# Kernel optimization log

Measured on AMD Instinct MI355X. Metric: run time of the kernel, lower is better.

The kernel has to match this reference:

```python
import jax, jax.numpy as jnp
import numpy as np

# DeepSeek-V3 MLA attention (q_lora_rank > 0 path), sdpa attn_type (causal)
B, S, DIM = 2, 2048, 2048
NH = 16
Q_LORA = 1536
KV_LORA = 512
NOPE = 128
ROPE = 64
VH = 128
QK_HD = NOPE + ROPE  # 192
EPS = 1e-6
SCALE = QK_HD ** -0.5
ROPE_THETA = 10000.0


def _freqs(seqlen, dim, base):
    f = 1.0 / base ** (np.arange(0, dim, 2, dtype=np.float32) / dim)
    ang = np.outer(np.arange(seqlen, dtype=np.float32), f)
    return jnp.asarray(np.cos(ang)), jnp.asarray(np.sin(ang))


def rmsnorm(x, w, eps=EPS):
    var = jnp.mean(jnp.square(x), axis=-1, keepdims=True)
    return x * jax.lax.rsqrt(var + eps) * w


def apply_rope(x, cos, sin):
    # x: [b, s, h, d]; cos/sin: [s, d//2]; interleaved complex pairs (x[2i], x[2i+1])
    xr, xi = x[..., 0::2], x[..., 1::2]
    c = cos[None, :, None, :]
    s = sin[None, :, None, :]
    yr = xr * c - xi * s
    yi = xr * s + xi * c
    return jnp.stack([yr, yi], axis=-1).reshape(x.shape)


def setup_inputs() -> dict:
    key = jax.random.key(0)
    ks = jax.random.split(key, 7)
    std = 0.02
    x = jax.random.normal(ks[0], (B, S, DIM), dtype=jnp.float32)
    cos, sin = _freqs(S, ROPE, ROPE_THETA)
    return {
        "x": x,
        "freqs_cos": cos,
        "freqs_sin": sin,
        "wq_a": jax.random.normal(ks[1], (DIM, Q_LORA), dtype=jnp.float32) * std,
        "q_norm_w": jnp.ones((Q_LORA,), dtype=jnp.float32),
        "wq_b": jax.random.normal(ks[2], (Q_LORA, NH * QK_HD), dtype=jnp.float32) * std,
        "wkv_a": jax.random.normal(ks[3], (DIM, KV_LORA + ROPE), dtype=jnp.float32) * std,
        "kv_norm_w": jnp.ones((KV_LORA,), dtype=jnp.float32),
        "wkv_b": jax.random.normal(ks[4], (KV_LORA, NH * (NOPE + VH)), dtype=jnp.float32) * std,
        "wo": jax.random.normal(ks[5], (NH * VH, DIM), dtype=jnp.float32) * std,
    }


def reference(x, freqs_cos, freqs_sin, wq_a, q_norm_w, wq_b, wkv_a, kv_norm_w, wkv_b, wo):
    b, s, _ = x.shape
    # low-rank Q projection: wq_a -> RMSNorm -> wq_b
    q = rmsnorm(x @ wq_a, q_norm_w) @ wq_b
    q = q.reshape(b, s, NH, QK_HD)
    q_nope, q_pe = q[..., :NOPE], q[..., NOPE:]
    q_pe = apply_rope(q_pe, freqs_cos, freqs_sin)
    q = jnp.concatenate([q_nope, q_pe], axis=-1)
    # low-rank KV: wkv_a -> split latent / rope part
    kv = x @ wkv_a
    kv_lat, k_pe = kv[..., :KV_LORA], kv[..., KV_LORA:]
    k_pe = apply_rope(k_pe[:, :, None, :], freqs_cos, freqs_sin)  # [b,s,1,ROPE]
    kv = rmsnorm(kv_lat, kv_norm_w) @ wkv_b
    kv = kv.reshape(b, s, NH, NOPE + VH)
    k_nope, v = kv[..., :NOPE], kv[..., NOPE:]
    k = jnp.concatenate([k_nope, jnp.broadcast_to(k_pe, (b, s, NH, ROPE))], axis=-1)
    # attention [b,h,s,d]
    q = q.transpose(0, 2, 1, 3)
    k = k.transpose(0, 2, 1, 3)
    v = v.transpose(0, 2, 1, 3)
    scores = jnp.einsum("bhqd,bhkd->bhqk", q, k) * SCALE
    causal = jnp.tril(jnp.ones((s, s), dtype=bool))
    scores = jnp.where(causal[None, None], scores, jnp.finfo(scores.dtype).min)
    probs = jax.nn.softmax(scores, axis=-1)
    out = jnp.einsum("bhqk,bhkd->bhqd", probs, v)
    out = out.transpose(0, 2, 1, 3).reshape(b, s, NH * VH)
    return out @ wo
```

## Files before the change

kernel.cpp:

```cpp
#include <hip/hip_runtime.h>
#include <cstdint>
#include <cstddef>

typedef __attribute__((ext_vector_type(8))) short bf16x8;
typedef __attribute__((ext_vector_type(4))) float f32x4;
typedef __attribute__((ext_vector_type(16))) float f32x16;

#define S_LEN 2048
#define SCALE2 0.10411754f

__device__ __forceinline__ ushort f2bf(float f) {
  uint32_t u = __float_as_uint(f);
  u = (u + 0x7FFFu + ((u >> 16) & 1u)) >> 16;
  return (ushort)u;
}
__device__ __forceinline__ float bf2f(ushort u) {
  return __uint_as_float(((uint32_t)u) << 16);
}

typedef __attribute__((address_space(1))) void GV;
typedef __attribute__((address_space(3))) void LV;
__device__ __forceinline__ void gload16(const void* g, void* l) {
  __builtin_amdgcn_global_load_lds((GV*)g, (LV*)l, 16, 0, 0);
}

__device__ __forceinline__ void store_out(float* p, float v) { *p = v; }
__device__ __forceinline__ void store_out(ushort* p, float v) { *p = f2bf(v); }

__global__ void k_pre(const float* __restrict__ s0, const float* __restrict__ s1,
                      const float* __restrict__ s2, const float* __restrict__ s3,
                      const float* __restrict__ s4,
                      ushort* __restrict__ d0, ushort* __restrict__ d1,
                      ushort* __restrict__ d2, ushort* __restrict__ d3,
                      ushort* __restrict__ d4,
                      const float* __restrict__ x, ushort* __restrict__ xb) {
  int id = blockIdx.x;
  if (id >= 14976) {
    int ft = threadIdx.y * 32 + threadIdx.x;
    int i = (id - 14976) * 256 + ft;
    const int n4 = 4096 * 2048 / 4, stride = 2048 * 256;
    for (; i < n4; i += stride) {
      float4 v = reinterpret_cast<const float4*>(x)[i];
      ushort4 o;
      o.x = f2bf(v.x); o.y = f2bf(v.y); o.z = f2bf(v.z); o.w = f2bf(v.w);
      reinterpret_cast<ushort4*>(xb)[i] = o;
    }
    return;
  }
  __shared__ float tile[32][33];
  const float* in; ushort* out; int R, C, gx, lid;
  if (id < 3072)        { in = s0; out = d0; R = 2048; C = 1536; gx = 48;  lid = id; }
  else if (id < 4224)   { in = s1; out = d1; R = 2048; C = 576;  gx = 18;  lid = id - 3072; }
  else if (id < 8832)   { in = s2; out = d2; R = 1536; C = 3072; gx = 96;  lid = id - 4224; }
  else if (id < 10880)  { in = s3; out = d3; R = 512;  C = 4096; gx = 128; lid = id - 8832; }
  else                  { in = s4; out = d4; R = 2048; C = 2048; gx = 64;  lid = id - 10880; }
  int c0 = (lid % gx) * 32, r0 = (lid / gx) * 32;
  int tx = threadIdx.x, ty = threadIdx.y;
#pragma unroll
  for (int i = 0; i < 32; i += 8) {
    int r = r0 + ty + i, c = c0 + tx;
    if (r < R && c < C) tile[ty + i][tx] = in[(size_t)r * C + c];
  }
  __syncthreads();
#pragma unroll
  for (int i = 0; i < 32; i += 8) {
    int c = c0 + ty + i, r = r0 + tx;
    if (r < R && c < C) out[(size_t)c * R + r] = f2bf(tile[tx][ty + i]);
  }
}

template <typename OUT>
__global__ __launch_bounds__(256) void k_gemm(const ushort* __restrict__ A,
                                              const ushort* __restrict__ Bt,
                                              OUT* __restrict__ C, int K, int Nreal) {
  __shared__ ushort As[128 * 72];
  __shared__ ushort Bs[128 * 72];
  const int t = threadIdx.x, lane = t & 63, w = t >> 6;
  const int nwg = gridDim.x * gridDim.y;
  const int wg = blockIdx.y * gridDim.x + blockIdx.x;
  const int swz = (wg & 7) * (nwg >> 3) + (wg >> 3);
  const int m0 = (swz / gridDim.x) * 128, n0 = (swz % gridDim.x) * 128;
  const int wm = (w >> 1) * 64, wn = (w & 1) * 64;
  const int g = lane >> 4, q = lane & 15;
  f32x4 acc[4][4] = {};
  for (int kt = 0; kt < K; kt += 64) {
#pragma unroll
    for (int it = 0; it < 5; ++it) {
      int ii = it * 4 + w;
      if (ii < 18) {
        unsigned s = ii * 64 + lane;
        int r = s / 9, e = s - r * 9;
        int cg = e ^ ((r >> 3) & 7);
        if (cg > 7) cg = 0;
        gload16(A + (size_t)(m0 + r) * K + kt + cg * 8, (char*)As + ii * 1024);
        gload16(Bt + (size_t)(n0 + r) * K + kt + cg * 8, (char*)Bs + ii * 1024);
      }
    }
    asm volatile("s_waitcnt vmcnt(0)" ::: "memory");
    __syncthreads();
#pragma unroll
    for (int kh = 0; kh < 2; ++kh) {
      bf16x8 af[4], bfr[4];
#pragma unroll
      for (int mi = 0; mi < 4; mi++) {
        int row = wm + 16 * mi + q;
        int rx = (row >> 3) & 7;
        af[mi] = *(const bf16x8*)(As + row * 72 + (((kh * 4 + g) ^ rx) << 3));
      }
#pragma unroll
      for (int ni = 0; ni < 4; ni++) {
        int row = wn + 16 * ni + q;
        int rx = (row >> 3) & 7;
        bfr[ni] = *(const bf16x8*)(Bs + row * 72 + (((kh * 4 + g) ^ rx) << 3));
      }
#pragma unroll
      for (int mi = 0; mi < 4; mi++)
#pragma unroll
        for (int ni = 0; ni < 4; ni++)
          acc[mi][ni] = __builtin_amdgcn_mfma_f32_16x16x32_bf16(af[mi], bfr[ni], acc[mi][ni], 0, 0, 0);
    }
    __syncthreads();
  }
#pragma unroll
  for (int mi = 0; mi < 4; mi++)
#pragma unroll
    for (int ni = 0; ni < 4; ni++) {
      int col = n0 + wn + 16 * ni + q;
      if (col < Nreal) {
        int row = m0 + wm + 16 * mi + 4 * g;
#pragma unroll
        for (int r = 0; r < 4; r++)
          store_out(&C[(size_t)(row + r) * Nreal + col], acc[mi][ni][r]);
      }
    }
}

__global__ __launch_bounds__(512, 1) void k_gemm_qkv256(
    const ushort* __restrict__ A1, const ushort* __restrict__ Bt1,
    ushort* __restrict__ C1,
    const float* __restrict__ cosT, const float* __restrict__ sinT,
    const ushort* __restrict__ A2, const ushort* __restrict__ Bt2,
    ushort* __restrict__ kbuf, ushort* __restrict__ vT) {
  __shared__ __align__(16) char lds[2][4][18432];
  const int t = threadIdx.x, lane = t & 63, w = t >> 6;
  const int q = lane & 15, g = lane >> 4;
  const int wm = w >> 2, wn = w & 3;
  const int id = blockIdx.x;
  const bool seg1 = (id < 192);
  const ushort* A  = seg1 ? A1 : A2;
  const ushort* Bt = seg1 ? Bt1 : Bt2;
  const int K   = seg1 ? 1536 : 512;
  const int gx  = seg1 ? 12 : 16;
  const int nwg = seg1 ? 192 : 256;
  const int wg  = seg1 ? id : id - 192;
  const int swz = (wg & 7) * (nwg >> 3) + (wg >> 3);
  const int m0 = (swz / gx) * 256, n0 = (swz % gx) * 256;
  const int nt = K >> 6;

  auto stageTile = [&](int kt, int p) {
#pragma unroll
    for (int it = 0; it < 9; ++it) {
      int u = it * 512 + (w << 6);
      int hh = u / 1152;
      int s0 = u - hh * 1152;
      int s = s0 + lane;
      int r = s / 9, c = s - r * 9;
      if (c > 7) c = 0;
      const ushort* src = (hh < 2) ? (A + (size_t)(m0 + (hh << 7) + r) * K)
                                   : (Bt + (size_t)(n0 + ((hh - 2) << 7) + r) * K);
      gload16(src + kt * 64 + c * 8, &lds[p][hh][s0 * 16]);
    }
  };

  f32x4 acc[8][4] = {};
  stageTile(0, 0);
  asm volatile("" ::: "memory");
  stageTile(1, 1);

  for (int kt = 0; kt < nt; ++kt) {
    const int p = kt & 1;
    if (kt == 0 || kt + 1 >= nt) asm volatile("s_waitcnt vmcnt(0)" ::: "memory");
    else                         asm volatile("s_waitcnt vmcnt(9)" ::: "memory");
    __builtin_amdgcn_s_barrier();
    asm volatile("" ::: "memory");
    const char* LA = &lds[p][wm][0];
    const char* LB = &lds[p][2 + (wn >> 1)][0];
    const int brow0 = (wn & 1) * 64;
    bf16x8 bfr[4][2];
#pragma unroll
    for (int ni = 0; ni < 4; ++ni) {
      bfr[ni][0] = *(const bf16x8*)(LB + (brow0 + ni * 16 + q) * 144 + 16 * g);
      bfr[ni][1] = *(const bf16x8*)(LB + (brow0 + ni * 16 + q) * 144 + 64 + 16 * g);
    }
    __builtin_amdgcn_s_setprio(1);
#pragma unroll
    for (int mi = 0; mi < 8; ++mi) {
      bf16x8 a0 = *(const bf16x8*)(LA + (mi * 16 + q) * 144 + 16 * g);
      bf16x8 a1 = *(const bf16x8*)(LA + (mi * 16 + q) * 144 + 64 + 16 * g);
#pragma unroll
      for (int ni = 0; ni < 4; ++ni)
        acc[mi][ni] = __builtin_amdgcn_mfma_f32_16x16x32_bf16(a0, bfr[ni][0], acc[mi][ni], 0, 0, 0);
#pragma unroll
      for (int ni = 0; ni < 4; ++ni)
        acc[mi][ni] = __builtin_amdgcn_mfma_f32_16x16x32_bf16(a1, bfr[ni][1], acc[mi][ni], 0, 0, 0);
    }
    __builtin_amdgcn_s_setprio(0);
    asm volatile("s_waitcnt lgkmcnt(0)" ::: "memory");
    __builtin_amdgcn_s_barrier();
    asm volatile("" ::: "memory");
    if (kt + 2 < nt) stageTile(kt + 2, p);
  }

  if (seg1) {
#pragma unroll
    for (int mi = 0; mi < 8; ++mi)
#pragma unroll
      for (int ni = 0; ni < 4; ++ni) {
        int col = n0 + wn * 64 + ni * 16 + q;
        int hoff = col % 192;
        int row = m0 + wm * 128 + mi * 16 + 4 * g;
        if (hoff < 128) {
#pragma unroll
          for (int r = 0; r < 4; r++)
            C1[(size_t)(row + r) * 3072 + col] = f2bf(acc[mi][ni][r]);
        } else {
          int i = (hoff - 128) >> 1;
#pragma unroll
          for (int r = 0; r < 4; r++) {
            int s2 = (row + r) & 2047;
            float c = cosT[s2 * 32 + i], sn = sinT[s2 * 32 + i];
            float v = acc[mi][ni][r];
            float pv = __shfl_xor(v, 1);
            float res = (q & 1) ? (pv * sn + v * c) : (v * c - pv * sn);
            C1[(size_t)(row + r) * 3072 + col] = f2bf(res);
          }
        }
      }
  } else {
#pragma unroll
    for (int mi = 0; mi < 8; ++mi)
#pragma unroll
      for (int ni = 0; ni < 4; ++ni) {
        int col = n0 + wn * 64 + ni * 16 + q;
        int hh = col >> 8, jj = col & 255;
        int row0 = m0 + wm * 128 + mi * 16 + 4 * g;
#pragma unroll
        for (int r = 0; r < 4; r++) {
          int tok = row0 + r;
          int bb = tok >> 11, ss = tok & 2047;
          ushort v = f2bf(acc[mi][ni][r]);
          if (jj < 128)
            kbuf[((size_t)(bb * 16 + hh) * 2048 + ss) * 192 + jj] = v;
          else
            vT[((size_t)(bb * 16 + hh) * 128 + (jj - 128)) * 2048 + ss] = v;
        }
      }
  }
}

__global__ void k_norms(const ushort* __restrict__ cqkv, const float* __restrict__ qnw,
                        const float* __restrict__ kvnw,
                        const float* __restrict__ cosT, const float* __restrict__ sinT,
                        ushort* __restrict__ cqn, ushort* __restrict__ ckvn,
                        ushort* __restrict__ kbuf) {
  __shared__ float red[4];
  int id = blockIdx.x;
  if (id < 4096) {
    int row = id;
    const ushort* x = cqkv + (size_t)row * 2112;
    ushort* o = cqn + (size_t)row * 1536;
    float ss = 0.f;
    for (int i = threadIdx.x; i < 1536; i += 256) { float v = bf2f(x[i]); ss += v * v; }
#pragma unroll
    for (int m = 1; m < 64; m <<= 1) ss += __shfl_xor(ss, m);
    if ((threadIdx.x & 63) == 0) red[threadIdx.x >> 6] = ss;
    __syncthreads();
    float tot = red[0] + red[1] + red[2] + red[3];
    float sc = rsqrtf(tot / 1536.f + 1e-6f);
    for (int i = threadIdx.x; i < 1536; i += 256) o[i] = f2bf(bf2f(x[i]) * sc * qnw[i]);
  } else {
    int tok = id - 4096, b = tok >> 11, s = tok & 2047;
    const ushort* x = cqkv + (size_t)tok * 2112 + 1536;
    float ss = 0.f;
    for (int i = threadIdx.x; i < 512; i += 256) { float v = bf2f(x[i]); ss += v * v; }
#pragma unroll
    for (int m = 1; m < 64; m <<= 1) ss += __shfl_xor(ss, m);
    if ((threadIdx.x & 63) == 0) red[threadIdx.x >> 6] = ss;
    __syncthreads();
    float tot = red[0] + red[1] + red[2] + red[3];
    float sc = rsqrtf(tot / 512.f + 1e-6f);
    for (int i = threadIdx.x; i < 512; i += 256) ckvn[(size_t)tok * 512 + i] = f2bf(bf2f(x[i]) * sc * kvnw[i]);
    if (threadIdx.x < 32) {
      int i = threadIdx.x;
      float xr = bf2f(x[512 + 2 * i]), xi = bf2f(x[512 + 2 * i + 1]);
      float c = cosT[s * 32 + i], sn = sinT[s * 32 + i];
      uint32_t lo = f2bf(xr * c - xi * sn);
      uint32_t hi = f2bf(xr * sn + xi * c);
      uint32_t pk = lo | (hi << 16);
#pragma unroll
      for (int h = 0; h < 16; ++h)
        *(uint32_t*)(kbuf + ((size_t)(b * 16 + h) * 2048 + s) * 192 + 128 + 2 * i) = pk;
    }
  }
}

__global__ __launch_bounds__(256, 2) void k_attn10(const ushort* __restrict__ qb,
                                                   const ushort* __restrict__ kb,
                                                   const ushort* __restrict__ vT,
                                                   ushort* __restrict__ aout) {
  const int id = blockIdx.x;
  const int qt = (id < 256) ? (15 - (id >> 5)) : ((id - 256) >> 5);
  const int bh = id & 31;
  const int h = bh & 15, b = bh >> 4;

  const int t = threadIdx.x, lane = t & 63, w = t >> 6;
  const int lq = lane & 31, hi = lane >> 5;
  const int kx = (lq >> 3) & 3;

  __shared__ ushort Ks[64 * 200];
  __shared__ ushort Vs[128 * 72];

  const ushort* kh = kb + (size_t)(b * 16 + h) * (2048 * 192);
  const ushort* vh = vT + (size_t)(b * 16 + h) * (128 * 2048);

  auto stage = [&](int k0) {
#pragma unroll
    for (int it = 0; it < 7; ++it) {
      int ii = it * 4 + w;
      if (ii < 25) {
        unsigned s = ii * 64 + lane;
        int r = s / 25, e = s - r * 25;
        int cg = e ^ ((r >> 3) & 3);
        if (cg > 23) cg = 0;
        gload16(kh + (size_t)(k0 + r) * 192 + cg * 8, (char*)Ks + ii * 1024);
      }
    }
#pragma unroll
    for (int it = 0; it < 5; ++it) {
      int ii = it * 4 + w;
      if (ii < 18) {
        unsigned s = ii * 64 + lane;
        int r = s / 9, e = s - r * 9;
        int cg = e ^ ((r >> 3) & 7);
        if (cg > 7) cg = 0;
        gload16(vh + (size_t)r * 2048 + k0 + cg * 8, (char*)Vs + ii * 1024);
      }
    }
  };

  const int q0 = qt * 128;
  const int q0w = q0 + 32 * w;
  const int qg = q0w + lq;
  const int nkt = qt * 2 + 2;

  bf16x8 qf[12];
  {
    const ushort* qp = qb + ((size_t)(b * 2048 + qg) * 16 + h) * 192 + 8 * hi;
#pragma unroll
    for (int s = 0; s < 12; ++s) qf[s] = *(const bf16x8*)(qp + 16 * s);
  }

  f32x16 oacc[4];
#pragma unroll
  for (int db = 0; db < 4; ++db)
#pragma unroll
    for (int r = 0; r < 16; ++r) oacc[db][r] = 0.f;
  float m = -1e30f, l = 0.f;

  for (int kt = 0; kt < nkt; ++kt) {
    const int k0 = kt * 64;
    stage(k0);
    asm volatile("s_waitcnt vmcnt(0)" ::: "memory");
    __syncthreads();
    if (k0 <= q0w + 31) {
      f32x16 sA, sB;
#pragma unroll
      for (int r = 0; r < 16; ++r) { sA[r] = 0.f; sB[r] = 0.f; }
      __builtin_amdgcn_s_setprio(1);
#pragma unroll
      for (int s = 0; s < 12; ++s) {
        int ch = ((2 * s + hi) ^ kx) << 3;
        bf16x8 kfA = *(const bf16x8*)(Ks + lq * 200 + ch);
        bf16x8 kfB = *(const bf16x8*)(Ks + (lq + 32) * 200 + ch);
        sA = __builtin_amdgcn_mfma_f32_32x32x16_bf16(kfA, qf[s], sA, 0, 0, 0);
        sB = __builtin_amdgcn_mfma_f32_32x32x16_bf16(kfB, qf[s], sB, 0, 0, 0);
      }
      __builtin_amdgcn_s_setprio(0);
      float svA[16], svB[16];
#pragma unroll
      for (int r = 0; r < 16; ++r) { svA[r] = sA[r]; svB[r] = sB[r]; }
      if (k0 + 63 > q0w) {
#pragma unroll
        for (int r = 0; r < 16; ++r) {
          int kk = (r & 3) + 8 * (r >> 2) + 4 * hi;
          if (k0 + kk > qg) svA[r] = -1e30f;
          if (k0 + 32 + kk > qg) svB[r] = -1e30f;
        }
      }
      float pmax = fmaxf(svA[0], svB[0]);
#pragma unroll
      for (int r = 1; r < 16; ++r) pmax = fmaxf(pmax, fmaxf(svA[r], svB[r]));
      pmax = fmaxf(pmax, __shfl_xor(pmax, 32));
      float smax = pmax * SCALE2;
      if (!__all(smax - m <= 8.0f)) {
        float mnew = fmaxf(m, smax);
        float a = exp2f(m - mnew);
        l *= a;
#pragma unroll
        for (int db = 0; db < 4; ++db)
#pragma unroll
          for (int r = 0; r < 16; ++r) oacc[db][r] *= a;
        m = mnew;
      }
      float eA[16], eB[16]; float sum = 0.f;
#pragma unroll
      for (int r = 0; r < 16; ++r) {
        eA[r] = exp2f(svA[r] * SCALE2 - m);
        eB[r] = exp2f(svB[r] * SCALE2 - m);
        sum += eA[r] + eB[r];
      }
      sum += __shfl_xor(sum, 32);
      l += sum;
      uint32_t pkA[8], pkB[8];
#pragma unroll
      for (int i = 0; i < 8; ++i) {
        pkA[i] = (uint32_t)f2bf(eA[2 * i]) | ((uint32_t)f2bf(eA[2 * i + 1]) << 16);
        pkB[i] = (uint32_t)f2bf(eB[2 * i]) | ((uint32_t)f2bf(eB[2 * i + 1]) << 16);
      }
      uint32_t swA[8], swB[8];
#pragma unroll
      for (int i = 0; i < 8; ++i) {
        swA[i] = (uint32_t)__shfl_xor((int)pkA[i], 32);
        swB[i] = (uint32_t)__shfl_xor((int)pkB[i], 32);
      }
      union { uint32_t u[4]; bf16x8 v; } pA0, pA1, pB0, pB1;
      pA0.u[0] = hi ? swA[2] : pkA[0];
      pA0.u[1] = hi ? swA[3] : pkA[1];
      pA0.u[2] = hi ? pkA[2] : swA[0];
      pA0.u[3] = hi ? pkA[3] : swA[1];
      pA1.u[0] = hi ? swA[6] : pkA[4];
      pA1.u[1] = hi ? swA[7] : pkA[5];
      pA1.u[2] = hi ? pkA[6] : swA[4];
      pA1.u[3] = hi ? pkA[7] : swA[5];
      pB0.u[0] = hi ? swB[2] : pkB[0];
      pB0.u[1] = hi ? swB[3] : pkB[1];
      pB0.u[2] = hi ? pkB[2] : swB[0];
      pB0.u[3] = hi ? pkB[3] : swB[1];
      pB1.u[0] = hi ? swB[6] : pkB[4];
      pB1.u[1] = hi ? swB[7] : pkB[5];
      pB1.u[2] = hi ? pkB[6] : swB[4];
      pB1.u[3] = hi ? pkB[7] : swB[5];
      __builtin_amdgcn_s_setprio(1);
#pragma unroll
      for (int db = 0; db < 4; ++db) {
        const int d = 32 * db + lq;
        const int vx = (d >> 3) & 7;
        const ushort* vr = Vs + d * 72;
        bf16x8 vf0 = *(const bf16x8*)(vr + (((0 + hi) ^ vx) << 3));
        bf16x8 vf1 = *(const bf16x8*)(vr + (((2 + hi) ^ vx) << 3));
        bf16x8 vf2 = *(const bf16x8*)(vr + (((4 + hi) ^ vx) << 3));
        bf16x8 vf3 = *(const bf16x8*)(vr + (((6 + hi) ^ vx) << 3));
        oacc[db] = __builtin_amdgcn_mfma_f32_32x32x16_bf16(vf0, pA0.v, oacc[db], 0, 0, 0);
        oacc[db] = __builtin_amdgcn_mfma_f32_32x32x16_bf16(vf1, pA1.v, oacc[db], 0, 0, 0);
        oacc[db] = __builtin_amdgcn_mfma_f32_32x32x16_bf16(vf2, pB0.v, oacc[db], 0, 0, 0);
        oacc[db] = __builtin_amdgcn_mfma_f32_32x32x16_bf16(vf3, pB1.v, oacc[db], 0, 0, 0);
      }
      __builtin_amdgcn_s_setprio(0);
    }
    asm volatile("s_waitcnt lgkmcnt(0)" ::: "memory");
    __syncthreads();
  }

  float inv = 1.f / l;
  ushort* op = aout + ((size_t)(b * 2048 + qg)) * 2048 + h * 128 + 4 * hi;
#pragma unroll
  for (int db = 0; db < 4; ++db)
#pragma unroll
    for (int i = 0; i < 8; ++i) {
      uint32_t u = (uint32_t)f2bf(oacc[db][2 * i] * inv) |
                   ((uint32_t)f2bf(oacc[db][2 * i + 1] * inv) << 16);
      int dbase = 32 * db + (i & 1) * 2 + (i >> 1) * 8;
      *(uint32_t*)(op + dbase) = u;
    }
}

extern "C" void kernel_launch(void* const* d_in, const int* in_sizes, int n_in,
                              void* d_out, int out_size, void* d_ws, size_t ws_size,
                              hipStream_t stream) {
  const float* x = (const float*)d_in[0];
  const float* fcos = (const float*)d_in[1];
  const float* fsin = (const float*)d_in[2];
  const float* wq_a = (const float*)d_in[3];
  const float* qnw = (const float*)d_in[4];
  const float* wq_b = (const float*)d_in[5];
  const float* wkv_a = (const float*)d_in[6];
  const float* kvnw = (const float*)d_in[7];
  const float* wkv_b = (const float*)d_in[8];
  const float* wo = (const float*)d_in[9];
  float* out = (float*)d_out;

  char* ws = (char*)d_ws;
  size_t off = 0;
  auto alloc = [&](size_t bytes) -> char* {
    char* p = ws + off;
    off += (bytes + 255) & ~(size_t)255;
    return p;
  };
  ushort* xb     = (ushort*)alloc(4096ull * 2048 * 2);
  ushort* wqkv_t = (ushort*)alloc(2176ull * 2048 * 2);
  ushort* wqb_t  = (ushort*)alloc(3072ull * 1536 * 2);
  ushort* wkvb_t = (ushort*)alloc(4096ull * 512 * 2);
  ushort* wo_t   = (ushort*)alloc(2048ull * 2048 * 2);
  ushort* cqkv   = (ushort*)alloc(4096ull * 2112 * 2);
  ushort* cqn    = (ushort*)alloc(4096ull * 1536 * 2);
  ushort* ckvn   = (ushort*)alloc(4096ull * 512 * 2);
  ushort* kbuf   = (ushort*)alloc(2ull * 16 * 2048 * 192 * 2);
  ushort* qbuf   = (ushort*)alloc(4096ull * 3072 * 2);
  ushort* aout   = xb;
  ushort* vT     = cqkv;

  k_pre<<<17024, dim3(32, 8), 0, stream>>>(
      wq_a, wkv_a, wq_b, wkv_b, wo,
      wqkv_t, wqkv_t + 1536ull * 2048, wqb_t, wkvb_t, wo_t,
      x, xb);

  k_gemm<ushort><<<dim3(17, 32), 256, 0, stream>>>(xb, wqkv_t, cqkv, 2048, 2112);

  k_norms<<<8192, 256, 0, stream>>>(cqkv, qnw, kvnw, fcos, fsin, cqn, ckvn, kbuf);

  k_gemm_qkv256<<<448, 512, 0, stream>>>(cqn, wqb_t, qbuf, fcos, fsin,
                                         ckvn, wkvb_t, kbuf, vT);

  k_attn10<<<dim3(512), 256, 0, stream>>>(qbuf, kbuf, vT, aout);

  k_gemm<float><<<dim3(16, 32), 256, 0, stream>>>(aout, wo_t, out, 2048, 2048);
}
```

Measured before the change: 329.5 us.

## Double-buffer LDS tiles in generic GEMM to overlap global loads with MFMA

The generic k_gemm kernel now keeps two LDS buffers for A and B and issues the loads for tile kt+2 right after computing tile kt. A partial vmcnt wait replaces the full drain, so global-to-LDS transfers can overlap with MFMA work. LDS use per block doubles, which may lower occupancy. The vmcnt(8) count must match the number of loads issued per stage, or the kernel could read tiles before they arrive.

```diff
diff --git a/kernel.cpp b/kernel.cpp
--- a/kernel.cpp
+++ b/kernel.cpp
@@ -73,8 +73,8 @@
 __global__ __launch_bounds__(256) void k_gemm(const ushort* __restrict__ A,
                                               const ushort* __restrict__ Bt,
                                               OUT* __restrict__ C, int K, int Nreal) {
-  __shared__ ushort As[128 * 72];
-  __shared__ ushort Bs[128 * 72];
+  __shared__ ushort As[2][128 * 72];
+  __shared__ ushort Bs[2][128 * 72];
   const int t = threadIdx.x, lane = t & 63, w = t >> 6;
   const int nwg = gridDim.x * gridDim.y;
   const int wg = blockIdx.y * gridDim.x + blockIdx.x;
@@ -82,8 +82,9 @@
   const int m0 = (swz / gridDim.x) * 128, n0 = (swz % gridDim.x) * 128;
   const int wm = (w >> 1) * 64, wn = (w & 1) * 64;
   const int g = lane >> 4, q = lane & 15;
-  f32x4 acc[4][4] = {};
-  for (int kt = 0; kt < K; kt += 64) {
+  const int nt = K >> 6;
+
+  auto stage = [&](int kt, int p) {
 #pragma unroll
     for (int it = 0; it < 5; ++it) {
       int ii = it * 4 + w;
@@ -92,12 +93,23 @@
         int r = s / 9, e = s - r * 9;
         int cg = e ^ ((r >> 3) & 7);
         if (cg > 7) cg = 0;
-        gload16(A + (size_t)(m0 + r) * K + kt + cg * 8, (char*)As + ii * 1024);
-        gload16(Bt + (size_t)(n0 + r) * K + kt + cg * 8, (char*)Bs + ii * 1024);
-      }
-    }
-    asm volatile("s_waitcnt vmcnt(0)" ::: "memory");
-    __syncthreads();
+        gload16(A + (size_t)(m0 + r) * K + kt * 64 + cg * 8, (char*)&As[p][0] + ii * 1024);
+        gload16(Bt + (size_t)(n0 + r) * K + kt * 64 + cg * 8, (char*)&Bs[p][0] + ii * 1024);
+      }
+    }
+  };
+
+  f32x4 acc[4][4] = {};
+  stage(0, 0);
+  asm volatile("" ::: "memory");
+  stage(1, 1);
+
+  for (int kt = 0; kt < nt; ++kt) {
+    const int p = kt & 1;
+    if (kt == 0 || kt + 1 >= nt) asm volatile("s_waitcnt vmcnt(0)" ::: "memory");
+    else                         asm volatile("s_waitcnt vmcnt(8)" ::: "memory");
+    __builtin_amdgcn_s_barrier();
+    asm volatile("" ::: "memory");
 #pragma unroll
     for (int kh = 0; kh < 2; ++kh) {
       bf16x8 af[4], bfr[4];
@@ -105,13 +117,13 @@
       for (int mi = 0; mi < 4; mi++) {
         int row = wm + 16 * mi + q;
         int rx = (row >> 3) & 7;
-        af[mi] = *(const bf16x8*)(As + row * 72 + (((kh * 4 + g) ^ rx) << 3));
+        af[mi] = *(const bf16x8*)(&As[p][0] + row * 72 + (((kh * 4 + g) ^ rx) << 3));
       }
 #pragma unroll
       for (int ni = 0; ni < 4; ni++) {
         int row = wn + 16 * ni + q;
         int rx = (row >> 3) & 7;
-        bfr[ni] = *(const bf16x8*)(Bs + row * 72 + (((kh * 4 + g) ^ rx) << 3));
+        bfr[ni] = *(const bf16x8*)(&Bs[p][0] + row * 72 + (((kh * 4 + g) ^ rx) << 3));
       }
 #pragma unroll
       for (int mi = 0; mi < 4; mi++)
@@ -119,8 +131,12 @@
         for (int ni = 0; ni < 4; ni++)
           acc[mi][ni] = __builtin_amdgcn_mfma_f32_16x16x32_bf16(af[mi], bfr[ni], acc[mi][ni], 0, 0, 0);
     }
-    __syncthreads();
-  }
+    asm volatile("s_waitcnt lgkmcnt(0)" ::: "memory");
+    __builtin_amdgcn_s_barrier();
+    asm volatile("" ::: "memory");
+    if (kt + 2 < nt) stage(kt + 2, p);
+  }
+
 #pragma unroll
   for (int mi = 0; mi < 4; mi++)
 #pragma unroll
```

Result: slower. 349.6 us (+6.1%).
